# Optimization experiments

Hardware: AMD Instinct MI355X
Metric: run time of the kernel (lower is better)

## Reference

```python
import jax, jax.numpy as jnp
import numpy as np

C = 64          # channels
HEADS = 4       # num_heads -> head_dim = 16
HID = int(C * 2.66)  # 170, GDFN hidden channels
B, H, W = 2, 256, 256


def conv1x1(x, w):
    # x: (b,c,h,w), w: (o,c) -> pointwise conv, no bias
    return jnp.einsum('bchw,oc->bohw', x, w)


def dwconv3x3(x, w):
    # depthwise 3x3, SAME padding; w: (C,1,3,3)
    return jax.lax.conv_general_dilated(
        x, w, window_strides=(1, 1), padding='SAME',
        feature_group_count=x.shape[1],
        dimension_numbers=('NCHW', 'OIHW', 'NCHW'))


def layer_norm_c(x, w, b):
    # torch: LayerNorm over channel dim of (b, hw, c), eps=1e-5
    mu = x.mean(axis=1, keepdims=True)
    var = ((x - mu) ** 2).mean(axis=1, keepdims=True)
    xn = (x - mu) / jnp.sqrt(var + 1e-5)
    return xn * w[None, :, None, None] + b[None, :, None, None]


def l2norm(x):
    # F.normalize(dim=-1), eps=1e-12
    n = jnp.sqrt(jnp.sum(x * x, axis=-1, keepdims=True))
    return x / jnp.maximum(n, 1e-12)


def mdta(x, temp, w_qkv, w_qkv_dw, w_po, w_kv, w_kv_dw, w_pof):
    b, c, h, w_ = x.shape
    d = c // HEADS
    qkv = dwconv3x3(conv1x1(x, w_qkv), w_qkv_dw)
    q, k, v = jnp.split(qkv, 3, axis=1)
    rs = lambda t: t.reshape(b, HEADS, d, h * w_)
    q, k, v = l2norm(rs(q)), l2norm(rs(k)), rs(v)
    # channel attention: (b,heads,d,d), softmax over last dim
    attn = jax.nn.softmax(jnp.einsum('bhdn,bhen->bhde', q, k) * temp, axis=-1)
    out = conv1x1(jnp.einsum('bhde,bhen->bhdn', attn, v).reshape(b, c, h, w_), w_po)
    # second gated branch: kv from `out`, reuse attn (qf/kf/attnf are dead code in source)
    kvf = dwconv3x3(conv1x1(out, w_kv), w_kv_dw)
    _kf, vf = jnp.split(kvf, 2, axis=1)
    vf = rs(vf)
    outf = conv1x1(jnp.einsum('bhde,bhen->bhdn', attn, vf).reshape(b, c, h, w_), w_pof)
    return outf


def gdfn(x, w_in, w_dw, w_out):
    x12 = dwconv3x3(conv1x1(x, w_in), w_dw)
    x1, x2 = jnp.split(x12, 2, axis=1)
    return conv1x1(jax.nn.gelu(x1, approximate=False) * x2, w_out)


def setup_inputs() -> dict:
    key = jax.random.key(0)
    ks = jax.random.split(key, 10)
    s = 0.05
    return {
        'x': jax.random.normal(ks[0], (B, C, H, W), jnp.float32),
        'n1_w': jnp.ones((C,), jnp.float32),
        'n1_b': jnp.zeros((C,), jnp.float32),
        'temp': jnp.ones((1, HEADS, 1, 1), jnp.float32),
        'w_qkv': jax.random.normal(ks[1], (3 * C, C), jnp.float32) * s,
        'w_qkv_dw': jax.random.normal(ks[2], (3 * C, 1, 3, 3), jnp.float32) * s,
        'w_po': jax.random.normal(ks[3], (C, C), jnp.float32) * s,
        'w_kv': jax.random.normal(ks[4], (2 * C, C), jnp.float32) * s,
        'w_kv_dw': jax.random.normal(ks[5], (2 * C, 1, 3, 3), jnp.float32) * s,
        'w_pof': jax.random.normal(ks[6], (C, C), jnp.float32) * s,
        'n2_w': jnp.ones((C,), jnp.float32),
        'n2_b': jnp.zeros((C,), jnp.float32),
        'w_in': jax.random.normal(ks[7], (2 * HID, C), jnp.float32) * s,
        'w_dw': jax.random.normal(ks[8], (2 * HID, 1, 3, 3), jnp.float32) * s,
        'w_out': jax.random.normal(ks[9], (C, HID), jnp.float32) * s,
    }


def reference(x, n1_w, n1_b, temp, w_qkv, w_qkv_dw, w_po, w_kv, w_kv_dw, w_pof,
              n2_w, n2_b, w_in, w_dw, w_out):
    x = x + mdta(layer_norm_c(x, n1_w, n1_b), temp,
                 w_qkv, w_qkv_dw, w_po, w_kv, w_kv_dw, w_pof)
    x = x + gdfn(layer_norm_c(x, n2_w, n2_b), w_in, w_dw, w_out)
    return x
```

## Files before the change

### kernel.cpp

```cpp
#include <hip/hip_runtime.h>
#include <hip/hip_bf16.h>
#include <math.h>

#define NPB 65536
#define BATCH 2
#define NTOT (BATCH * NPB)

typedef unsigned short u16;
typedef __attribute__((ext_vector_type(8))) short short8;
typedef __attribute__((ext_vector_type(4))) float f32x4;


__device__ __forceinline__ float bf2f(u16 u) {
  union { unsigned u; float f; } v; v.u = ((unsigned)u) << 16; return v.f;
}
__device__ __forceinline__ u16 f2bf(float f) {
  union { float f; unsigned u; } v; v.f = f;
  unsigned r = v.u + 0x7FFFu + ((v.u >> 16) & 1u);
  return (u16)(r >> 16);
}
__device__ __forceinline__ unsigned pk2(float a, float b) {
  return (unsigned)f2bf(a) | ((unsigned)f2bf(b) << 16);
}
__device__ __forceinline__ f32x4 mm(short8 a, short8 b, f32x4 c) {
  return __builtin_amdgcn_mfma_f32_16x16x32_bf16(a, b, c, 0, 0, 0);
}
__device__ __forceinline__ short8 ldfrag(const u16* F, int frag, int l) {
  return *reinterpret_cast<const short8*>(F + ((size_t)frag * 64 + l) * 8);
}
__device__ __forceinline__ void st4(u16* p, f32x4 c) {
  uint2 v; v.x = pk2(c[0], c[1]); v.y = pk2(c[2], c[3]);
  *reinterpret_cast<uint2*>(p) = v;
}

__global__ __launch_bounds__(64) void k_wprep(
    const float* __restrict__ wqkv, const float* __restrict__ win,
    const float* __restrict__ wout, u16* __restrict__ WQf,
    u16* __restrict__ WIf, u16* __restrict__ WOf)
{
  const int f = blockIdx.x;
  const int l = threadIdx.x;
  const int fr = l & 15, fq = l >> 4;
  short8 v;
  u16* dst;
  if (f < 24) {
    const int t = f >> 1, kh = f & 1;
    const int row = t * 16 + fr;
#pragma unroll
    for (int j = 0; j < 8; ++j)
      v[j] = (short)f2bf(wqkv[(size_t)row * 64 + kh * 32 + fq * 8 + j]);
    dst = WQf + ((size_t)f * 64 + l) * 8;
  } else if (f < 68) {
    const int fi = f - 24;
    const int g = fi >> 1, kh = fi & 1;
    const int half = g / 11, t = g % 11;
    const int col = half * 176 + t * 16 + fr;
    const int row = col < 170 ? col : (col < 176 ? -1 : (col < 346 ? col - 6 : -1));
#pragma unroll
    for (int j = 0; j < 8; ++j)
      v[j] = (row < 0) ? (short)0
             : (short)f2bf(win[(size_t)row * 64 + kh * 32 + fq * 8 + j]);
    dst = WIf + ((size_t)fi * 64 + l) * 8;
  } else {
    const int fi = f - 68;
    const int t = fi / 6, kh = fi % 6;
    const int row = t * 16 + fr;
#pragma unroll
    for (int j = 0; j < 8; ++j) {
      const int k = kh * 32 + fq * 8 + j;
      v[j] = (k < 170) ? (short)f2bf(wout[(size_t)row * 170 + k]) : (short)0;
    }
    dst = WOf + ((size_t)fi * 64 + l) * 8;
  }
  *reinterpret_cast<short8*>(dst) = v;
}

__global__ __launch_bounds__(256, 4) void k_ln1(
    const float* __restrict__ x, const float* __restrict__ n1w,
    const float* __restrict__ n1b, u16* __restrict__ Y1)
{
  const int n = blockIdx.x * 256 + threadIdx.x;
  const int b = blockIdx.y;
  const size_t pix = (size_t)b * NPB + n;
  const float* xb = x + ((size_t)b * 64) * NPB + n;
  float y[64];
  float mu = 0.f;
#pragma unroll
  for (int c = 0; c < 64; ++c) { y[c] = xb[(size_t)c * NPB]; mu += y[c]; }
  mu *= (1.f / 64.f);
  float var = 0.f;
#pragma unroll
  for (int c = 0; c < 64; ++c) { float d = y[c] - mu; var = fmaf(d, d, var); }
  const float rstd = rsqrtf(var * (1.f / 64.f) + 1e-5f);
#pragma unroll
  for (int c = 0; c < 64; ++c) y[c] = (y[c] - mu) * rstd * n1w[c] + n1b[c];
#pragma unroll
  for (int cb = 0; cb < 4; ++cb) {
    u16* dst = Y1 + ((size_t)cb * NTOT + pix) * 16;
    uint4 v0, v1;
    v0.x = pk2(y[cb*16+0],  y[cb*16+1]);  v0.y = pk2(y[cb*16+2],  y[cb*16+3]);
    v0.z = pk2(y[cb*16+4],  y[cb*16+5]);  v0.w = pk2(y[cb*16+6],  y[cb*16+7]);
    v1.x = pk2(y[cb*16+8],  y[cb*16+9]);  v1.y = pk2(y[cb*16+10], y[cb*16+11]);
    v1.z = pk2(y[cb*16+12], y[cb*16+13]); v1.w = pk2(y[cb*16+14], y[cb*16+15]);
    *reinterpret_cast<uint4*>(dst) = v0;
    *reinterpret_cast<uint4*>(dst + 8) = v1;
  }
}

__global__ __launch_bounds__(256, 2) void g_qkvp(
    const u16* __restrict__ Y1, const u16* __restrict__ WQf,
    u16* __restrict__ qkvp)
{
  const int l = threadIdx.x & 63, fr = l & 15, fq = l >> 4;
  const int wv = blockIdx.x * 4 + (threadIdx.x >> 6);
  const int nw = gridDim.x * 4;
  short8 A[12][2];
#pragma unroll
  for (int t = 0; t < 12; ++t)
#pragma unroll
    for (int kh = 0; kh < 2; ++kh) A[t][kh] = ldfrag(WQf, t * 2 + kh, l);
  const size_t hof = (size_t)(fq & 1) * 8;
  for (int tile = wv; tile < 8192; tile += nw) {
    const size_t n = (size_t)tile * 16 + fr;
    const short8 b0 = *reinterpret_cast<const short8*>(
        Y1 + (((size_t)(fq >> 1)) * NTOT + n) * 16 + hof);
    const short8 b1 = *reinterpret_cast<const short8*>(
        Y1 + (((size_t)(2 + (fq >> 1))) * NTOT + n) * 16 + hof);
    f32x4 c[12];
#pragma unroll
    for (int t = 0; t < 12; ++t) c[t] = f32x4{0.f, 0.f, 0.f, 0.f};
#pragma unroll
    for (int t = 0; t < 12; ++t) c[t] = mm(A[t][0], b0, c[t]);
#pragma unroll
    for (int t = 0; t < 12; ++t) c[t] = mm(A[t][1], b1, c[t]);
#pragma unroll
    for (int t = 0; t < 12; ++t)
      st4(qkvp + ((size_t)t * NTOT + n) * 16 + fq * 4, c[t]);
  }
}

template<int CH, bool GATE, int STRIP>
__global__ __launch_bounds__(256, 2) void k_dwr(
    const u16* __restrict__ in, u16* __restrict__ out,
    const float* __restrict__ wdw, int wofs)
{
  typedef short __attribute__((ext_vector_type(CH))) shortC;
  constexpr int NPL = GATE ? 2 : 1;
  constexpr int LPP = 16 / CH;
  constexpr int NX  = 256 / LPP;
  constexpr int XC  = 256 / NX;
  const int t = threadIdx.x;
  const int sub = t % LPP, xi = t / LPP;
  const int q = blockIdx.x / XC, xc = blockIdx.x % XC;
  const int strip = blockIdx.y, b = blockIdx.z;
  const int x = xc * NX + xi;
  const int y0 = strip * STRIP;
  const int e0 = sub * CH;
  const int c0 = q * 16 + e0;

  const u16* pin[NPL];
  pin[0] = in + ((size_t)q * NTOT + (size_t)b * NPB) * 16 + e0;
  if (GATE)
    pin[NPL - 1] = in + ((size_t)(11 + q) * NTOT + (size_t)b * NPB) * 16 + e0;

  float w[NPL][9][CH];
#pragma unroll
  for (int pl = 0; pl < NPL; ++pl)
#pragma unroll
    for (int ch = 0; ch < CH; ++ch) {
      const int c = c0 + ch;
      int row; bool valid;
      if (GATE) { valid = c < 170; row = pl * 170 + c; }
      else { valid = true; row = wofs + c; }
#pragma unroll
      for (int tap = 0; tap < 9; ++tap)
        w[pl][tap][ch] = valid ? wdw[(size_t)row * 9 + tap] : 0.f;
    }

  auto LD = [&](const u16* p, int yy, int xx) -> shortC {
    shortC v;
#pragma unroll
    for (int j = 0; j < CH; ++j) v[j] = 0;
    if ((unsigned)yy < 256u && (unsigned)xx < 256u)
      v = *reinterpret_cast<const shortC*>(p + (size_t)(yy * 256 + xx) * 16);
    return v;
  };

  shortC r[NPL][3][3];
#pragma unroll
  for (int pl = 0; pl < NPL; ++pl) {
    r[pl][0][0] = LD(pin[pl], y0 - 1, x - 1);
    r[pl][0][1] = LD(pin[pl], y0 - 1, x);
    r[pl][0][2] = LD(pin[pl], y0 - 1, x + 1);
    r[pl][1][0] = LD(pin[pl], y0, x - 1);
    r[pl][1][1] = LD(pin[pl], y0, x);
    r[pl][1][2] = LD(pin[pl], y0, x + 1);
  }

#pragma unroll 2
  for (int yy = 0; yy < STRIP; ++yy) {
    const int y = y0 + yy;
#pragma unroll
    for (int pl = 0; pl < NPL; ++pl) {
      r[pl][2][0] = LD(pin[pl], y + 1, x - 1);
      r[pl][2][1] = LD(pin[pl], y + 1, x);
      r[pl][2][2] = LD(pin[pl], y + 1, x + 1);
    }
    float acc[NPL][CH];
#pragma unroll
    for (int pl = 0; pl < NPL; ++pl)
#pragma unroll
      for (int ch = 0; ch < CH; ++ch) acc[pl][ch] = 0.f;
#pragma unroll
    for (int pl = 0; pl < NPL; ++pl)
#pragma unroll
      for (int ky = 0; ky < 3; ++ky)
#pragma unroll
        for (int kx = 0; kx < 3; ++kx)
#pragma unroll
          for (int ch = 0; ch < CH; ++ch)
            acc[pl][ch] = fmaf(w[pl][ky * 3 + kx][ch],
                               bf2f((u16)r[pl][ky][kx][ch]), acc[pl][ch]);

    float v[CH];
#pragma unroll
    for (int ch = 0; ch < CH; ++ch) {
      if (GATE) {
        const float a = acc[0][ch];
        v[ch] = 0.5f * a * (1.f + erff(a * 0.70710678118f)) * acc[NPL - 1][ch];
      } else {
        v[ch] = acc[0][ch];
      }
    }
    u16* po = out + ((size_t)q * NTOT + (size_t)b * NPB +
                     (size_t)(y * 256 + x)) * 16 + e0;
    if constexpr (CH == 4) {
      uint2 o; o.x = pk2(v[0], v[1]); o.y = pk2(v[2], v[3]);
      *reinterpret_cast<uint2*>(po) = o;
    } else {
      uint4 o;
      o.x = pk2(v[0], v[1]); o.y = pk2(v[2], v[3]);
      o.z = pk2(v[4], v[5]); o.w = pk2(v[6], v[7]);
      *reinterpret_cast<uint4*>(po) = o;
    }
#pragma unroll
    for (int pl = 0; pl < NPL; ++pl)
#pragma unroll
      for (int dx = 0; dx < 3; ++dx) {
        r[pl][0][dx] = r[pl][1][dx];
        r[pl][1][dx] = r[pl][2][dx];
      }
  }
}

__global__ __launch_bounds__(256, 2) void k_gram_p(
    const u16* __restrict__ qkv, float* __restrict__ part)
{
  __shared__ __align__(16) u16 lds[32][520];
  const int chunk = blockIdx.x, h = blockIdx.y, b = blockIdx.z;
  const int t = threadIdx.x;
#pragma unroll
  for (int i = 0; i < 2; ++i) {
    const int p = t + i * 256;
    const size_t pix = (size_t)b * NPB + chunk * 512 + p;
    const u16* srcq = qkv + ((size_t)h * NTOT + pix) * 16;
    const u16* srck = qkv + ((size_t)(4 + h) * NTOT + pix) * 16;
    const short8 q0 = *reinterpret_cast<const short8*>(srcq);
    const short8 q1 = *reinterpret_cast<const short8*>(srcq + 8);
    const short8 k0 = *reinterpret_cast<const short8*>(srck);
    const short8 k1 = *reinterpret_cast<const short8*>(srck + 8);
#pragma unroll
    for (int j = 0; j < 8; ++j) {
      lds[j][p] = (u16)q0[j];  lds[8 + j][p] = (u16)q1[j];
      lds[16 + j][p] = (u16)k0[j]; lds[24 + j][p] = (u16)k1[j];
    }
  }
  __syncthreads();
  const int w = t >> 6, l = t & 63, fr = l & 15, fq = l >> 4;
  if (w >= 3) return;
  float* pp = part + ((size_t)((b * 4 + h) * 128) + chunk) * 288;
  const int rowA = (w == 2) ? 16 + fr : fr;
  const int rowB = (w == 0) ? 16 + fr : rowA;
  f32x4 acc = {0.f, 0.f, 0.f, 0.f};
#pragma unroll
  for (int kt = 0; kt < 16; ++kt) {
    const short8 a  = *reinterpret_cast<const short8*>(&lds[rowA][kt * 32 + fq * 8]);
    const short8 bb = *reinterpret_cast<const short8*>(&lds[rowB][kt * 32 + fq * 8]);
    acc = mm(a, bb, acc);
  }
  if (w == 0) {
#pragma unroll
    for (int r = 0; r < 4; ++r) pp[(fq * 4 + r) * 16 + fr] = acc[r];
  } else if ((fr >> 2) == fq) {
    pp[(w == 1 ? 256 : 272) + fr] = acc[fr & 3];
  }
}

__global__ __launch_bounds__(320) void k_gram_red(
    const float* __restrict__ part, float* __restrict__ G,
    float* __restrict__ Sq, float* __restrict__ Sk)
{
  const int bh = blockIdx.x;
  const int t = threadIdx.x;
  if (t >= 288) return;
  const float* p = part + (size_t)bh * 128 * 288 + t;
  float s = 0.f;
  for (int ch = 0; ch < 128; ++ch) s += p[(size_t)ch * 288];
  const int b = bh >> 2, h = bh & 3;
  if (t < 256) G[bh * 256 + t] = s;
  else if (t < 272) Sq[b * 64 + h * 16 + (t - 256)] = s;
  else Sk[b * 64 + h * 16 + (t - 272)] = s;
}

__global__ __launch_bounds__(256) void k_attn(
    const float* __restrict__ G, const float* __restrict__ Sq,
    const float* __restrict__ Sk, const float* __restrict__ temp,
    const float* __restrict__ wpo, const float* __restrict__ wkv,
    const float* __restrict__ wpof, u16* __restrict__ Pf,
    u16* __restrict__ M2f)
{
  __shared__ float attn[BATCH][4][16][16];
  __shared__ float M1[BATCH][64][64];
  __shared__ float rq[128], rk[128];
  const int t = threadIdx.x;
  if (t < 128) {
    rq[t] = 1.f / fmaxf(sqrtf(Sq[t]), 1e-12f);
    rk[t] = 1.f / fmaxf(sqrtf(Sk[t]), 1e-12f);
  }
  __syncthreads();
  if (t < 128) {
    const int b = t >> 6, h = (t >> 4) & 3, d = t & 15;
    const float tm = temp[h];
    const float* g = G + ((b * 4 + h) * 16 + d) * 16;
    const float rqd = rq[b * 64 + h * 16 + d];
    float L[16], mx = -1e30f;
#pragma unroll
    for (int e = 0; e < 16; ++e) {
      L[e] = g[e] * rqd * rk[b * 64 + h * 16 + e] * tm;
      mx = fmaxf(mx, L[e]);
    }
    float s = 0.f;
#pragma unroll
    for (int e = 0; e < 16; ++e) { L[e] = expf(L[e] - mx); s += L[e]; }
    const float inv = 1.f / s;
#pragma unroll
    for (int e = 0; e < 16; ++e) attn[b][h][d][e] = L[e] * inv;
  }
  __syncthreads();
  for (int s0 = 0; s0 < 32; ++s0) {
    const int idx = t * 32 + s0;
    const int b = idx >> 12, o = (idx >> 6) & 63, c = idx & 63;
    const int h = c >> 4, e = c & 15;
    float a = 0.f;
#pragma unroll
    for (int d = 0; d < 16; ++d) a = fmaf(wpo[o * 64 + h * 16 + d], attn[b][h][d][e], a);
    M1[b][o][c] = a;
  }
  __syncthreads();
  for (int it = 0; it < 4; ++it) {
    const int idx = it * 256 + t;
    const int l = idx & 63;
    const int fi = idx >> 6;
    const int b = fi >> 3, tt = (fi >> 1) & 3, kh = fi & 1;
    const int fr = l & 15, fq = l >> 4;
    const int o = tt * 16 + fr;
    short8 pv, mv;
#pragma unroll
    for (int j = 0; j < 8; ++j) {
      const int c = kh * 32 + fq * 8 + j;
      const int h = c >> 4, e = c & 15;
      float a2 = 0.f;
#pragma unroll
      for (int d = 0; d < 16; ++d)
        a2 = fmaf(wpof[o * 64 + h * 16 + d], attn[b][h][d][e], a2);
      mv[j] = (short)f2bf(a2);
      float a = 0.f;
      for (int jj = 0; jj < 64; ++jj)
        a = fmaf(wkv[(64 + o) * 64 + jj], M1[b][jj][c], a);
      pv[j] = (short)f2bf(a);
    }
    *reinterpret_cast<short8*>(Pf + ((size_t)fi * 64 + l) * 8) = pv;
    *reinterpret_cast<short8*>(M2f + ((size_t)fi * 64 + l) * 8) = mv;
  }
}

__global__ __launch_bounds__(256, 2) void g_pv(
    const u16* __restrict__ qkv, const u16* __restrict__ Pf,
    u16* __restrict__ vfp)
{
  const int l = threadIdx.x & 63, fr = l & 15, fq = l >> 4;
  const int wv = blockIdx.x * 4 + (threadIdx.x >> 6);
  const int nw = gridDim.x * 4;
  const int b = blockIdx.z;
  short8 A[4][2];
#pragma unroll
  for (int t = 0; t < 4; ++t)
#pragma unroll
    for (int kh = 0; kh < 2; ++kh)
      A[t][kh] = ldfrag(Pf, (b * 4 + t) * 2 + kh, l);
  const size_t hof = (size_t)(fq & 1) * 8;
  for (int tile = wv; tile < 4096; tile += nw) {
    const size_t n = (size_t)b * NPB + (size_t)tile * 16 + fr;
    const short8 b0 = *reinterpret_cast<const short8*>(
        qkv + ((size_t)(8 + (fq >> 1)) * NTOT + n) * 16 + hof);
    const short8 b1 = *reinterpret_cast<const short8*>(
        qkv + ((size_t)(10 + (fq >> 1)) * NTOT + n) * 16 + hof);
    f32x4 c[4];
#pragma unroll
    for (int t = 0; t < 4; ++t) c[t] = f32x4{0.f, 0.f, 0.f, 0.f};
#pragma unroll
    for (int t = 0; t < 4; ++t) c[t] = mm(A[t][0], b0, c[t]);
#pragma unroll
    for (int t = 0; t < 4; ++t) c[t] = mm(A[t][1], b1, c[t]);
#pragma unroll
    for (int t = 0; t < 4; ++t)
      st4(vfp + ((size_t)t * NTOT + n) * 16 + fq * 4, c[t]);
  }
}

__global__ __launch_bounds__(256, 2) void g_x2ln(
    const u16* __restrict__ vf, const u16* __restrict__ M2f,
    const float* __restrict__ x, const float* __restrict__ n2w,
    const float* __restrict__ n2b, u16* __restrict__ X2,
    u16* __restrict__ Y2)
{
  const int l = threadIdx.x & 63, fr = l & 15, fq = l >> 4;
  const int wv = blockIdx.x * 4 + (threadIdx.x >> 6);
  const int nw = gridDim.x * 4;
  const int b = blockIdx.z;
  short8 A[4][2];
#pragma unroll
  for (int t = 0; t < 4; ++t)
#pragma unroll
    for (int kh = 0; kh < 2; ++kh)
      A[t][kh] = ldfrag(M2f, (b * 4 + t) * 2 + kh, l);
  const size_t hof = (size_t)(fq & 1) * 8;
  for (int tile = wv; tile < 4096; tile += nw) {
    const int pix0 = tile * 16;
    const size_t n = (size_t)b * NPB + pix0 + fr;
    const short8 b0 = *reinterpret_cast<const short8*>(
        vf + ((size_t)(fq >> 1) * NTOT + n) * 16 + hof);
    const short8 b1 = *reinterpret_cast<const short8*>(
        vf + ((size_t)(2 + (fq >> 1)) * NTOT + n) * 16 + hof);
    f32x4 c[4];
#pragma unroll
    for (int t = 0; t < 4; ++t) c[t] = f32x4{0.f, 0.f, 0.f, 0.f};
#pragma unroll
    for (int t = 0; t < 4; ++t) c[t] = mm(A[t][0], b0, c[t]);
#pragma unroll
    for (int t = 0; t < 4; ++t) c[t] = mm(A[t][1], b1, c[t]);
    const int pix = pix0 + fr;
#pragma unroll
    for (int t = 0; t < 4; ++t)
#pragma unroll
      for (int r = 0; r < 4; ++r)
        c[t][r] += x[((size_t)(b * 64 + t * 16 + fq * 4 + r)) * NPB + pix];
#pragma unroll
    for (int t = 0; t < 4; ++t)
      st4(X2 + ((size_t)t * NTOT + n) * 16 + fq * 4, c[t]);
    float s = 0.f;
#pragma unroll
    for (int t = 0; t < 4; ++t)
#pragma unroll
      for (int r = 0; r < 4; ++r) s += c[t][r];
    s += __shfl_xor(s, 16); s += __shfl_xor(s, 32);
    const float mu = s * (1.f / 64.f);
    float ss = 0.f;
#pragma unroll
    for (int t = 0; t < 4; ++t)
#pragma unroll
      for (int r = 0; r < 4; ++r) { float d = c[t][r] - mu; ss = fmaf(d, d, ss); }
    ss += __shfl_xor(ss, 16); ss += __shfl_xor(ss, 32);
    const float rstd = rsqrtf(ss * (1.f / 64.f) + 1e-5f);
#pragma unroll
    for (int t = 0; t < 4; ++t)
#pragma unroll
      for (int r = 0; r < 4; ++r) {
        const int oc = t * 16 + fq * 4 + r;
        c[t][r] = (c[t][r] - mu) * rstd * n2w[oc] + n2b[oc];
      }
#pragma unroll
    for (int t = 0; t < 4; ++t)
      st4(Y2 + ((size_t)t * NTOT + n) * 16 + fq * 4, c[t]);
  }
}

__global__ __launch_bounds__(256, 2) void g_win(
    const u16* __restrict__ Y2, const u16* __restrict__ WIf,
    u16* __restrict__ hpre)
{
  const int l = threadIdx.x & 63, fr = l & 15, fq = l >> 4;
  const int wv = blockIdx.x * 4 + (threadIdx.x >> 6);
  const int nw = gridDim.x * 4;
  const int half = wv & 1;
  short8 A[11][2];
#pragma unroll
  for (int t = 0; t < 11; ++t)
#pragma unroll
    for (int kh = 0; kh < 2; ++kh)
      A[t][kh] = ldfrag(WIf, (half * 11 + t) * 2 + kh, l);
  const size_t hof = (size_t)(fq & 1) * 8;
  for (int tile = wv >> 1; tile < 8192; tile += (nw >> 1)) {
    const size_t n = (size_t)tile * 16 + fr;
    const short8 b0 = *reinterpret_cast<const short8*>(
        Y2 + ((size_t)(fq >> 1) * NTOT + n) * 16 + hof);
    const short8 b1 = *reinterpret_cast<const short8*>(
        Y2 + ((size_t)(2 + (fq >> 1)) * NTOT + n) * 16 + hof);
    f32x4 c[11];
#pragma unroll
    for (int t = 0; t < 11; ++t) c[t] = f32x4{0.f, 0.f, 0.f, 0.f};
#pragma unroll
    for (int t = 0; t < 11; ++t) c[t] = mm(A[t][0], b0, c[t]);
#pragma unroll
    for (int t = 0; t < 11; ++t) c[t] = mm(A[t][1], b1, c[t]);
#pragma unroll
    for (int t = 0; t < 11; ++t)
      st4(hpre + ((size_t)(half * 11 + t) * NTOT + n) * 16 + fq * 4, c[t]);
  }
}

__global__ __launch_bounds__(256, 2) void g_out(
    const u16* __restrict__ hg, const u16* __restrict__ WOf,
    const u16* __restrict__ X2, float* __restrict__ out)
{
  const int l = threadIdx.x & 63, fr = l & 15, fq = l >> 4;
  const int wv = blockIdx.x * 4 + (threadIdx.x >> 6);
  const int nw = gridDim.x * 4;
  short8 A[4][6];
#pragma unroll
  for (int t = 0; t < 4; ++t)
#pragma unroll
    for (int kh = 0; kh < 6; ++kh)
      A[t][kh] = ldfrag(WOf, t * 6 + kh, l);
  const size_t hof = (size_t)(fq & 1) * 8;
  for (int tile = wv; tile < 8192; tile += nw) {
    const size_t n = (size_t)tile * 16 + fr;
    short8 bb[6];
#pragma unroll
    for (int kh = 0; kh < 6; ++kh) {
      int hb = kh * 2 + (fq >> 1);
      if (hb > 10) hb = 10;
      bb[kh] = *reinterpret_cast<const short8*>(
          hg + ((size_t)hb * NTOT + n) * 16 + hof);
    }
    f32x4 c[4];
#pragma unroll
    for (int t = 0; t < 4; ++t) c[t] = f32x4{0.f, 0.f, 0.f, 0.f};
#pragma unroll
    for (int kh = 0; kh < 6; ++kh)
#pragma unroll
      for (int t = 0; t < 4; ++t) c[t] = mm(A[t][kh], bb[kh], c[t]);
    const int b = (int)(n >> 16);
    const int pix = (int)(n & 65535);
#pragma unroll
    for (int t = 0; t < 4; ++t) {
      const uint2 xv = *reinterpret_cast<const uint2*>(
          X2 + ((size_t)t * NTOT + n) * 16 + fq * 4);
      const u16 h0 = (u16)(xv.x & 0xffff), h1 = (u16)(xv.x >> 16);
      const u16 h2 = (u16)(xv.y & 0xffff), h3 = (u16)(xv.y >> 16);
      const int ocb = b * 64 + t * 16 + fq * 4;
      out[((size_t)(ocb + 0)) * NPB + pix] = c[t][0] + bf2f(h0);
      out[((size_t)(ocb + 1)) * NPB + pix] = c[t][1] + bf2f(h1);
      out[((size_t)(ocb + 2)) * NPB + pix] = c[t][2] + bf2f(h2);
      out[((size_t)(ocb + 3)) * NPB + pix] = c[t][3] + bf2f(h3);
    }
  }
}

extern "C" void kernel_launch(void* const* d_in, const int* in_sizes, int n_in,
                              void* d_out, int out_size, void* d_ws, size_t ws_size,
                              hipStream_t stream)
{
  const float* x     = (const float*)d_in[0];
  const float* n1w   = (const float*)d_in[1];
  const float* n1b   = (const float*)d_in[2];
  const float* temp  = (const float*)d_in[3];
  const float* wqkv  = (const float*)d_in[4];
  const float* wqkvd = (const float*)d_in[5];
  const float* wpo   = (const float*)d_in[6];
  const float* wkv   = (const float*)d_in[7];
  const float* wkvd  = (const float*)d_in[8];
  const float* wpof  = (const float*)d_in[9];
  const float* n2w   = (const float*)d_in[10];
  const float* n2b   = (const float*)d_in[11];
  const float* win   = (const float*)d_in[12];
  const float* wdw   = (const float*)d_in[13];
  const float* wout  = (const float*)d_in[14];
  float* out = (float*)d_out;

  char* ws = (char*)d_ws;
  const size_t offA  = 0;
  const size_t offB  = 16777216;
  const size_t offC  = offB + 50331648;
  const size_t offHg = offC + 50331648;
  const size_t offX2 = offHg + 46137344 + 256;
  const size_t offSm = offX2 + 16777216;

  u16* Y1   = (u16*)(ws + offA);
  u16* VFP  = (u16*)(ws + offA);
  u16* Y2   = (u16*)(ws + offA);
  u16* QKVp = (u16*)(ws + offB);
  u16* VF   = (u16*)(ws + offB);
  u16* Hpre = (u16*)(ws + offB);
  u16* QKV  = (u16*)(ws + offC);
  u16* Hg   = (u16*)(ws + offHg);
  u16* X2   = (u16*)(ws + offX2);
  float* part = (float*)(ws + offSm);
  float* G    = (float*)(ws + offSm + 1179648);
  float* Sq   = (float*)(ws + offSm + 1179648 + 8192);
  float* Sk   = (float*)(ws + offSm + 1179648 + 8704);
  u16* Pf     = (u16*)(ws + offSm + 1179648 + 9216);
  u16* M2f    = (u16*)(ws + offSm + 1179648 + 25600);
  u16* WQf    = (u16*)(ws + offSm + 1179648 + 41984);
  u16* WIf    = (u16*)(ws + offSm + 1179648 + 66560);
  u16* WOf    = (u16*)(ws + offSm + 1179648 + 111616);

  k_wprep<<<dim3(92), 64, 0, stream>>>(wqkv, win, wout, WQf, WIf, WOf);
  k_ln1<<<dim3(NPB / 256, BATCH), 256, 0, stream>>>(x, n1w, n1b, Y1);
  g_qkvp<<<dim3(512), 256, 0, stream>>>(Y1, WQf, QKVp);
  k_dwr<8, false, 16><<<dim3(24, 16, BATCH), 256, 0, stream>>>(QKVp, QKV, wqkvd, 0);
  k_gram_p<<<dim3(128, 4, BATCH), 256, 0, stream>>>(QKV, part);
  k_gram_red<<<dim3(BATCH * 4), 320, 0, stream>>>(part, G, Sq, Sk);
  k_attn<<<dim3(1), 256, 0, stream>>>(G, Sq, Sk, temp, wpo, wkv, wpof, Pf, M2f);
  g_pv<<<dim3(256, 1, BATCH), 256, 0, stream>>>(QKV, Pf, VFP);
  k_dwr<8, false, 8><<<dim3(8, 32, BATCH), 256, 0, stream>>>(VFP, VF, wkvd, 64);
  g_x2ln<<<dim3(256, 1, BATCH), 256, 0, stream>>>(VF, M2f, x, n2w, n2b, X2, Y2);
  g_win<<<dim3(512), 256, 0, stream>>>(Y2, WIf, Hpre);
  k_dwr<4, true, 16><<<dim3(44, 16, BATCH), 256, 0, stream>>>(Hpre, Hg, wdw, 0);
  g_out<<<dim3(512), 256, 0, stream>>>(Hg, WOf, X2, out);
}
```

Baseline: 240.5 us.

## Restructure depthwise conv kernels for higher occupancy and tanh GELU gate

Replaces the generic depthwise 3x3 kernel with two specialised ones that use 4 channels per thread and allow 4 blocks per CU. Edge columns are handled by clamping addresses and zeroing weights instead of per-load bounds checks. The gated kernel now splits the two planes across lanes and combines them with a lane shuffle. Exact erf GELU is replaced by the tanh approximation, which adds numerical deviation from the reference's exact GELU.

After: 254.6 us. +5.8%, slower.

```diff
diff --git a/kernel.cpp b/kernel.cpp
--- a/kernel.cpp
+++ b/kernel.cpp
@@ -8,6 +8,7 @@
 
 typedef unsigned short u16;
 typedef __attribute__((ext_vector_type(8))) short short8;
+typedef __attribute__((ext_vector_type(4))) short short4v;
 typedef __attribute__((ext_vector_type(4))) float f32x4;
 
 
@@ -31,6 +32,12 @@
 __device__ __forceinline__ void st4(u16* p, f32x4 c) {
   uint2 v; v.x = pk2(c[0], c[1]); v.y = pk2(c[2], c[3]);
   *reinterpret_cast<uint2*>(p) = v;
+}
+__device__ __forceinline__ float gelu_t(float a) {
+  const float z = 0.7978845608f * fmaf(0.044715f * a, a * a, a);
+  const float e = __expf(2.f * z);
+  const float th = 1.f - 2.f / (e + 1.f);
+  return 0.5f * a * (1.f + th);
 }
 
 __global__ __launch_bounds__(64) void k_wprep(
@@ -139,117 +146,156 @@
   }
 }
 
-template<int CH, bool GATE, int STRIP>
-__global__ __launch_bounds__(256, 2) void k_dwr(
+template<int STRIP>
+__global__ __launch_bounds__(256, 4) void k_dwr4(
     const u16* __restrict__ in, u16* __restrict__ out,
     const float* __restrict__ wdw, int wofs)
 {
-  typedef short __attribute__((ext_vector_type(CH))) shortC;
-  constexpr int NPL = GATE ? 2 : 1;
-  constexpr int LPP = 16 / CH;
-  constexpr int NX  = 256 / LPP;
-  constexpr int XC  = 256 / NX;
   const int t = threadIdx.x;
-  const int sub = t % LPP, xi = t / LPP;
-  const int q = blockIdx.x / XC, xc = blockIdx.x % XC;
+  const int sub = t & 3, xi = t >> 2;
+  const int q = blockIdx.x >> 2, xc = blockIdx.x & 3;
   const int strip = blockIdx.y, b = blockIdx.z;
-  const int x = xc * NX + xi;
+  const int x = xc * 64 + xi;
   const int y0 = strip * STRIP;
-  const int e0 = sub * CH;
-  const int c0 = q * 16 + e0;
-
-  const u16* pin[NPL];
-  pin[0] = in + ((size_t)q * NTOT + (size_t)b * NPB) * 16 + e0;
-  if (GATE)
-    pin[NPL - 1] = in + ((size_t)(11 + q) * NTOT + (size_t)b * NPB) * 16 + e0;
-
-  float w[NPL][9][CH];
-#pragma unroll
-  for (int pl = 0; pl < NPL; ++pl)
-#pragma unroll
-    for (int ch = 0; ch < CH; ++ch) {
-      const int c = c0 + ch;
-      int row; bool valid;
-      if (GATE) { valid = c < 170; row = pl * 170 + c; }
-      else { valid = true; row = wofs + c; }
-#pragma unroll
-      for (int tap = 0; tap < 9; ++tap)
-        w[pl][tap][ch] = valid ? wdw[(size_t)row * 9 + tap] : 0.f;
-    }
-
-  auto LD = [&](const u16* p, int yy, int xx) -> shortC {
-    shortC v;
-#pragma unroll
-    for (int j = 0; j < CH; ++j) v[j] = 0;
-    if ((unsigned)yy < 256u && (unsigned)xx < 256u)
-      v = *reinterpret_cast<const shortC*>(p + (size_t)(yy * 256 + xx) * 16);
-    return v;
+  const int e0 = sub * 4;
+  const u16* pin = in + ((size_t)q * NTOT + (size_t)b * NPB) * 16 + e0;
+
+  float w[9][4];
+#pragma unroll
+  for (int ch = 0; ch < 4; ++ch) {
+    const int row = wofs + q * 16 + e0 + ch;
+#pragma unroll
+    for (int tap = 0; tap < 9; ++tap) w[tap][ch] = wdw[(size_t)row * 9 + tap];
+  }
+  if (x == 0) {
+#pragma unroll
+    for (int ky = 0; ky < 3; ++ky)
+#pragma unroll
+      for (int ch = 0; ch < 4; ++ch) w[ky * 3 + 0][ch] = 0.f;
+  }
+  if (x == 255) {
+#pragma unroll
+    for (int ky = 0; ky < 3; ++ky)
+#pragma unroll
+      for (int ch = 0; ch < 4; ++ch) w[ky * 3 + 2][ch] = 0.f;
+  }
+  const int xl = x > 0 ? x - 1 : x;
+  const int xr = x < 255 ? x + 1 : x;
+  const size_t oL = (size_t)xl * 16, oC = (size_t)x * 16, oR = (size_t)xr * 16;
+
+  short4v r[3][3];
+  auto LDROW = [&](int yy, short4v* d) {
+    if ((unsigned)yy < 256u) {
+      const u16* rp = pin + (size_t)yy * 4096;
+      d[0] = *reinterpret_cast<const short4v*>(rp + oL);
+      d[1] = *reinterpret_cast<const short4v*>(rp + oC);
+      d[2] = *reinterpret_cast<const short4v*>(rp + oR);
+    } else {
+      short4v z; z[0] = z[1] = z[2] = z[3] = 0;
+      d[0] = z; d[1] = z; d[2] = z;
+    }
   };
-
-  shortC r[NPL][3][3];
-#pragma unroll
-  for (int pl = 0; pl < NPL; ++pl) {
-    r[pl][0][0] = LD(pin[pl], y0 - 1, x - 1);
-    r[pl][0][1] = LD(pin[pl], y0 - 1, x);
-    r[pl][0][2] = LD(pin[pl], y0 - 1, x + 1);
-    r[pl][1][0] = LD(pin[pl], y0, x - 1);
-    r[pl][1][1] = LD(pin[pl], y0, x);
-    r[pl][1][2] = LD(pin[pl], y0, x + 1);
-  }
-
-#pragma unroll 2
+  LDROW(y0 - 1, r[0]);
+  LDROW(y0, r[1]);
+#pragma unroll 4
   for (int yy = 0; yy < STRIP; ++yy) {
     const int y = y0 + yy;
-#pragma unroll
-    for (int pl = 0; pl < NPL; ++pl) {
-      r[pl][2][0] = LD(pin[pl], y + 1, x - 1);
-      r[pl][2][1] = LD(pin[pl], y + 1, x);
-      r[pl][2][2] = LD(pin[pl], y + 1, x + 1);
-    }
-    float acc[NPL][CH];
-#pragma unroll
-    for (int pl = 0; pl < NPL; ++pl)
-#pragma unroll
-      for (int ch = 0; ch < CH; ++ch) acc[pl][ch] = 0.f;
-#pragma unroll
-    for (int pl = 0; pl < NPL; ++pl)
-#pragma unroll
-      for (int ky = 0; ky < 3; ++ky)
-#pragma unroll
-        for (int kx = 0; kx < 3; ++kx)
-#pragma unroll
-          for (int ch = 0; ch < CH; ++ch)
-            acc[pl][ch] = fmaf(w[pl][ky * 3 + kx][ch],
-                               bf2f((u16)r[pl][ky][kx][ch]), acc[pl][ch]);
-
-    float v[CH];
-#pragma unroll
-    for (int ch = 0; ch < CH; ++ch) {
-      if (GATE) {
-        const float a = acc[0][ch];
-        v[ch] = 0.5f * a * (1.f + erff(a * 0.70710678118f)) * acc[NPL - 1][ch];
-      } else {
-        v[ch] = acc[0][ch];
-      }
-    }
-    u16* po = out + ((size_t)q * NTOT + (size_t)b * NPB +
-                     (size_t)(y * 256 + x)) * 16 + e0;
-    if constexpr (CH == 4) {
+    LDROW(y + 1, r[2]);
+    float acc[4] = {0.f, 0.f, 0.f, 0.f};
+#pragma unroll
+    for (int ky = 0; ky < 3; ++ky)
+#pragma unroll
+      for (int kx = 0; kx < 3; ++kx)
+#pragma unroll
+        for (int ch = 0; ch < 4; ++ch)
+          acc[ch] = fmaf(w[ky * 3 + kx][ch], bf2f((u16)r[ky][kx][ch]), acc[ch]);
+    uint2 o; o.x = pk2(acc[0], acc[1]); o.y = pk2(acc[2], acc[3]);
+    *reinterpret_cast<uint2*>(
+        out + ((size_t)q * NTOT + (size_t)b * NPB + (size_t)(y * 256 + x)) * 16 + e0) = o;
+#pragma unroll
+    for (int j = 0; j < 3; ++j) { r[0][j] = r[1][j]; r[1][j] = r[2][j]; }
+  }
+}
+
+template<int STRIP>
+__global__ __launch_bounds__(256, 4) void k_dwg(
+    const u16* __restrict__ in, u16* __restrict__ out,
+    const float* __restrict__ wdw)
+{
+  const int t = threadIdx.x;
+  const int sub = t & 7, xi = t >> 3;
+  const int pl = sub >> 2, cs = sub & 3;
+  const int q = blockIdx.x >> 3, xc = blockIdx.x & 7;
+  const int strip = blockIdx.y, b = blockIdx.z;
+  const int x = xc * 32 + xi;
+  const int y0 = strip * STRIP;
+  const int e0 = cs * 4;
+  const u16* pin = in + ((size_t)(q + pl * 11) * NTOT + (size_t)b * NPB) * 16 + e0;
+
+  float w[9][4];
+#pragma unroll
+  for (int ch = 0; ch < 4; ++ch) {
+    const int c = q * 16 + e0 + ch;
+    const int row = pl * 170 + c;
+    const bool valid = c < 170;
+#pragma unroll
+    for (int tap = 0; tap < 9; ++tap)
+      w[tap][ch] = valid ? wdw[(size_t)row * 9 + tap] : 0.f;
+  }
+  if (x == 0) {
+#pragma unroll
+    for (int ky = 0; ky < 3; ++ky)
+#pragma unroll
+      for (int ch = 0; ch < 4; ++ch) w[ky * 3 + 0][ch] = 0.f;
+  }
+  if (x == 255) {
+#pragma unroll
+    for (int ky = 0; ky < 3; ++ky)
+#pragma unroll
+      for (int ch = 0; ch < 4; ++ch) w[ky * 3 + 2][ch] = 0.f;
+  }
+  const int xl = x > 0 ? x - 1 : x;
+  const int xr = x < 255 ? x + 1 : x;
+  const size_t oL = (size_t)xl * 16, oC = (size_t)x * 16, oR = (size_t)xr * 16;
+
+  short4v r[3][3];
+  auto LDROW = [&](int yy, short4v* d) {
+    if ((unsigned)yy < 256u) {
+      const u16* rp = pin + (size_t)yy * 4096;
+      d[0] = *reinterpret_cast<const short4v*>(rp + oL);
+      d[1] = *reinterpret_cast<const short4v*>(rp + oC);
+      d[2] = *reinterpret_cast<const short4v*>(rp + oR);
+    } else {
+      short4v z; z[0] = z[1] = z[2] = z[3] = 0;
+      d[0] = z; d[1] = z; d[2] = z;
+    }
+  };
+  LDROW(y0 - 1, r[0]);
+  LDROW(y0, r[1]);
+#pragma unroll 4
+  for (int yy = 0; yy < STRIP; ++yy) {
+    const int y = y0 + yy;
+    LDROW(y + 1, r[2]);
+    float acc[4] = {0.f, 0.f, 0.f, 0.f};
+#pragma unroll
+    for (int ky = 0; ky < 3; ++ky)
+#pragma unroll
+      for (int kx = 0; kx < 3; ++kx)
+#pragma unroll
+        for (int ch = 0; ch < 4; ++ch)
+          acc[ch] = fmaf(w[ky * 3 + kx][ch], bf2f((u16)r[ky][kx][ch]), acc[ch]);
+    float o0 = __shfl_xor(acc[0], 4), o1 = __shfl_xor(acc[1], 4);
+    float o2 = __shfl_xor(acc[2], 4), o3 = __shfl_xor(acc[3], 4);
+    if (pl == 0) {
+      float v[4];
+      v[0] = gelu_t(acc[0]) * o0; v[1] = gelu_t(acc[1]) * o1;
+      v[2] = gelu_t(acc[2]) * o2; v[3] = gelu_t(acc[3]) * o3;
       uint2 o; o.x = pk2(v[0], v[1]); o.y = pk2(v[2], v[3]);
-      *reinterpret_cast<uint2*>(po) = o;
-    } else {
-      uint4 o;
-      o.x = pk2(v[0], v[1]); o.y = pk2(v[2], v[3]);
-      o.z = pk2(v[4], v[5]); o.w = pk2(v[6], v[7]);
-      *reinterpret_cast<uint4*>(po) = o;
-    }
-#pragma unroll
-    for (int pl = 0; pl < NPL; ++pl)
-#pragma unroll
-      for (int dx = 0; dx < 3; ++dx) {
-        r[pl][0][dx] = r[pl][1][dx];
-        r[pl][1][dx] = r[pl][2][dx];
-      }
+      *reinterpret_cast<uint2*>(
+          out + ((size_t)q * NTOT + (size_t)b * NPB + (size_t)(y * 256 + x)) * 16 + e0) = o;
+    }
+#pragma unroll
+    for (int j = 0; j < 3; ++j) { r[0][j] = r[1][j]; r[1][j] = r[2][j]; }
   }
 }
 
@@ -618,14 +664,14 @@
   k_wprep<<<dim3(92), 64, 0, stream>>>(wqkv, win, wout, WQf, WIf, WOf);
   k_ln1<<<dim3(NPB / 256, BATCH), 256, 0, stream>>>(x, n1w, n1b, Y1);
   g_qkvp<<<dim3(512), 256, 0, stream>>>(Y1, WQf, QKVp);
-  k_dwr<8, false, 16><<<dim3(24, 16, BATCH), 256, 0, stream>>>(QKVp, QKV, wqkvd, 0);
+  k_dwr4<16><<<dim3(48, 16, BATCH), 256, 0, stream>>>(QKVp, QKV, wqkvd, 0);
   k_gram_p<<<dim3(128, 4, BATCH), 256, 0, stream>>>(QKV, part);
   k_gram_red<<<dim3(BATCH * 4), 320, 0, stream>>>(part, G, Sq, Sk);
   k_attn<<<dim3(1), 256, 0, stream>>>(G, Sq, Sk, temp, wpo, wkv, wpof, Pf, M2f);
   g_pv<<<dim3(256, 1, BATCH), 256, 0, stream>>>(QKV, Pf, VFP);
-  k_dwr<8, false, 8><<<dim3(8, 32, BATCH), 256, 0, stream>>>(VFP, VF, wkvd, 64);
+  k_dwr4<8><<<dim3(16, 32, BATCH), 256, 0, stream>>>(VFP, VF, wkvd, 64);
   g_x2ln<<<dim3(256, 1, BATCH), 256, 0, stream>>>(VF, M2f, x, n2w, n2b, X2, Y2);
   g_win<<<dim3(512), 256, 0, stream>>>(Y2, WIf, Hpre);
-  k_dwr<4, true, 16><<<dim3(44, 16, BATCH), 256, 0, stream>>>(Hpre, Hg, wdw, 0);
+  k_dwg<16><<<dim3(88, 16, BATCH), 256, 0, stream>>>(Hpre, Hg, wdw);
   g_out<<<dim3(512), 256, 0, stream>>>(Hg, WOf, X2, out);
 }
```
